# Performance work log

Measured on AMD Instinct MI355X. Metric: run time of the kernel, lower is better.

## Reference

```python
import jax, jax.numpy as jnp
import numpy as np

N = 100_000
E = 3_200_000
IN_DIM = 2
HID = 64
NUM_LAYERS = 3


def setup_inputs() -> dict:
    key = jax.random.key(0)
    ks = jax.random.split(key, 16)
    feat = jax.random.normal(ks[0], (N, IN_DIM), dtype=jnp.float32)
    src = jax.random.randint(ks[1], (E,), 0, N, dtype=jnp.int32)
    dst = jax.random.randint(ks[2], (E,), 0, N, dtype=jnp.int32)
    u_mask = jnp.zeros((N,), dtype=bool).at[jnp.arange(0, 10)].set(True)
    v_mask = jnp.zeros((N,), dtype=bool).at[jnp.arange(10, 20)].set(True)
    inp = {"feat": feat, "src": src, "dst": dst, "u_mask": u_mask, "v_mask": v_mask}
    dims = [IN_DIM] + [HID] * NUM_LAYERS
    ki = 3
    for l in range(NUM_LAYERS):
        d_in = dims[l]
        inp[f"W1_{l}"] = jax.random.normal(ks[ki], (d_in, HID), dtype=jnp.float32) * (1.0 / np.sqrt(d_in)); ki += 1
        inp[f"b1_{l}"] = jnp.zeros((HID,), dtype=jnp.float32)
        inp[f"W2_{l}"] = jax.random.normal(ks[ki], (HID, HID), dtype=jnp.float32) * (1.0 / np.sqrt(HID)); ki += 1
        inp[f"b2_{l}"] = jnp.zeros((HID,), dtype=jnp.float32)
    return inp


def _gin_layer(h, src, dst, W1, b1, W2, b2, n_nodes):
    # GINConv(sum, eps=0): h' = MLP(h + sum_{j->i} h_j)
    agg = jax.ops.segment_sum(h[src], dst, num_segments=n_nodes)  # [N, d]
    z = h + agg
    z = jax.nn.relu(z @ W1 + b1)
    z = z @ W2 + b2
    return jax.nn.relu(z)  # module applies relu after conv


def _masked_means(h, u_mask, v_mask):
    other_mask = ~(u_mask | v_mask)
    masks = jnp.stack([u_mask, v_mask, other_mask]).astype(h.dtype)  # [3, N]
    counts = masks.sum(axis=1)                                      # [3]
    sums = masks @ h                                                # [3, H]
    means = jnp.where(counts[:, None] > 0,
                      sums / jnp.maximum(counts, 1.0)[:, None],
                      jnp.zeros_like(sums))
    return means.reshape(-1)  # [3*H] = [h_u | h_v | h_other]


def reference(feat, src, dst, u_mask, v_mask,
              W1_0, b1_0, W2_0, b2_0,
              W1_1, b1_1, W2_1, b2_1,
              W1_2, b1_2, W2_2, b2_2):
    n_nodes = feat.shape[0]
    params = [(W1_0, b1_0, W2_0, b2_0), (W1_1, b1_1, W2_1, b2_1), (W1_2, b1_2, W2_2, b2_2)]
    h = feat
    parts = []
    for (W1, b1, W2, b2) in params:
        h = _gin_layer(h, src, dst, W1, b1, W2, b2, n_nodes)
        parts.append(_masked_means(h, u_mask, v_mask))
    return jnp.concatenate(parts)  # (num_layers * 3 * hidden_dim,)
```

## Files before the change

### kernel.cpp

```cpp
#include <hip/hip_runtime.h>

#define HID 64
#define G_LOG 7
#define G_SZ 128
#define NBKT_MAX 1024
#define STAGE_MAX 6144

typedef float f32x4 __attribute__((ext_vector_type(4)));
typedef short bf16x8 __attribute__((ext_vector_type(8)));

__device__ __forceinline__ float bf2f(unsigned int u) {
    union { unsigned int i; float f; } c; c.i = u << 16; return c.f;
}
__device__ __forceinline__ float bf2f_hi(unsigned int u) {
    union { unsigned int i; float f; } c; c.i = u & 0xFFFF0000u; return c.f;
}
__device__ __forceinline__ unsigned short f2bf(float f) {
    union { float f; unsigned int i; } c; c.f = f;
    unsigned int r = (c.i + 0x7FFFu + ((c.i >> 16) & 1u)) >> 16;
    return (unsigned short)r;
}
__device__ __forceinline__ unsigned int pack2(float a, float b) {
    return (unsigned int)f2bf(a) | ((unsigned int)f2bf(b) << 16);
}

__global__ void detect_mask_kernel(const unsigned char* __restrict__ u,
                                   int* __restrict__ flag)
{
    *flag = (u[1] != 0) ? 1 : 0;
}

__device__ __forceinline__ int mask_at(const void* m, int n, int is_u8)
{
    return is_u8 ? (((const unsigned char*)m)[n] != 0)
                 : (((const int*)m)[n] != 0);
}

__global__ __launch_bounds__(256) void count_masks_kernel(
    const void* __restrict__ u, const void* __restrict__ v,
    const int* __restrict__ flag, int* __restrict__ counts, int N)
{
    const int is_u8 = *flag;
    int tid = blockIdx.x * blockDim.x + threadIdx.x;
    int stride = gridDim.x * blockDim.x;
    int cu = 0, cv = 0, co = 0;
    for (int n = tid; n < N; n += stride) {
        int bu = mask_at(u, n, is_u8), bv = mask_at(v, n, is_u8);
        cu += bu; cv += bv; co += ((bu | bv) ^ 1);
    }
    atomicAdd(&counts[0], cu);
    atomicAdd(&counts[1], cv);
    atomicAdd(&counts[2], co);
}

__global__ __launch_bounds__(1024) void bucket_hist_kernel(
    const int* __restrict__ dst, int* __restrict__ bktCount, int E, int nbkt)
{
    __shared__ int lh[NBKT_MAX];
    const int bdim = blockDim.x;
    for (int i = threadIdx.x; i < nbkt; i += bdim) lh[i] = 0;
    __syncthreads();
    const int chunk = (E + gridDim.x - 1) / gridDim.x;
    const int c0 = blockIdx.x * chunk;
    const int c1 = min(E, c0 + chunk);
    for (int e = c0 + threadIdx.x; e < c1; e += bdim)
        atomicAdd(&lh[dst[e] >> G_LOG], 1);
    __syncthreads();
    for (int i = threadIdx.x; i < nbkt; i += bdim)
        if (lh[i]) atomicAdd(&bktCount[i], lh[i]);
}

__global__ __launch_bounds__(1024) void bucket_scan_kernel(
    const int* __restrict__ bktCount, int* __restrict__ bktBase,
    int* __restrict__ bktCursor, int nbkt)
{
    __shared__ int s[NBKT_MAX];
    const int t = threadIdx.x;
    int v = (t < nbkt) ? bktCount[t] : 0;
    s[t] = v;
    __syncthreads();
    for (int off = 1; off < NBKT_MAX; off <<= 1) {
        int x = (t >= off) ? s[t - off] : 0;
        __syncthreads();
        s[t] += x;
        __syncthreads();
    }
    if (t < nbkt) {
        int excl = s[t] - v;
        bktBase[t] = excl;
        bktCursor[t] = excl;
        if (t == nbkt - 1) bktBase[nbkt] = s[t];
    }
}

__global__ __launch_bounds__(1024) void binning_kernel(
    const int* __restrict__ src, const int* __restrict__ dst,
    int* __restrict__ bktCursor, unsigned int* __restrict__ packed,
    int E, int nbkt)
{
    __shared__ int lh[NBKT_MAX];
    __shared__ int lbase[NBKT_MAX];
    __shared__ int lcur[NBKT_MAX];
    const int bdim = blockDim.x;
    for (int i = threadIdx.x; i < nbkt; i += bdim) { lh[i] = 0; lcur[i] = 0; }
    __syncthreads();
    const int chunk = (E + gridDim.x - 1) / gridDim.x;
    const int c0 = blockIdx.x * chunk;
    const int c1 = min(E, c0 + chunk);
    for (int e = c0 + threadIdx.x; e < c1; e += bdim)
        atomicAdd(&lh[dst[e] >> G_LOG], 1);
    __syncthreads();
    for (int i = threadIdx.x; i < nbkt; i += bdim) {
        int h = lh[i];
        lbase[i] = h ? atomicAdd(&bktCursor[i], h) : 0;
    }
    __syncthreads();
    for (int e = c0 + threadIdx.x; e < c1; e += bdim) {
        int d = dst[e];
        int b = d >> G_LOG;
        int r = atomicAdd(&lcur[b], 1);
        packed[lbase[b] + r] =
            (unsigned int)src[e] | ((unsigned int)(d & (G_SZ - 1)) << 20);
    }
}

__global__ __launch_bounds__(512) void bucket_csr_kernel(
    const unsigned int* __restrict__ packed, const int* __restrict__ bktBase,
    int* __restrict__ row_ptr, int* __restrict__ csr_src, int N, int E)
{
    __shared__ int ncount[G_SZ];
    __shared__ int sc[G_SZ];
    __shared__ int ncur[G_SZ];
    __shared__ int stage[STAGE_MAX];
    const int b = blockIdx.x;
    const int t = threadIdx.x;
    const int bdim = blockDim.x;
    const int beg = bktBase[b], end = bktBase[b + 1];
    const int cnt = end - beg;

    if (t < G_SZ) ncount[t] = 0;
    __syncthreads();
    for (int i = beg + t; i < end; i += bdim)
        atomicAdd(&ncount[(packed[i] >> 20) & (G_SZ - 1)], 1);
    __syncthreads();
    if (t < G_SZ) sc[t] = ncount[t];
    __syncthreads();
    for (int off = 1; off < G_SZ; off <<= 1) {
        int x = 0;
        if (t < G_SZ && t >= off) x = sc[t - off];
        __syncthreads();
        if (t < G_SZ) sc[t] += x;
        __syncthreads();
    }
    if (t < G_SZ) {
        int excl = sc[t] - ncount[t];
        ncur[t] = excl;
        int node = (b << G_LOG) + t;
        if (node < N) row_ptr[node] = beg + excl;
    }
    if (b == 0 && t == 0) row_ptr[N] = E;
    __syncthreads();

    if (cnt <= STAGE_MAX) {
        for (int i = beg + t; i < end; i += bdim) {
            unsigned int p = packed[i];
            int dl = (p >> 20) & (G_SZ - 1);
            int r = atomicAdd(&ncur[dl], 1);
            stage[r] = (int)(p & 0xFFFFFu);
        }
        __syncthreads();
        for (int i = t; i < cnt; i += bdim) csr_src[beg + i] = stage[i];
    } else {
        for (int i = beg + t; i < end; i += bdim) {
            unsigned int p = packed[i];
            int dl = (p >> 20) & (G_SZ - 1);
            int r = atomicAdd(&ncur[dl], 1);
            csr_src[beg + r] = (int)(p & 0xFFFFFu);
        }
    }
}

__global__ __launch_bounds__(256) void gather64_kernel(
    const unsigned short* __restrict__ h, const int* __restrict__ row_ptr,
    const int* __restrict__ csr_src, unsigned short* __restrict__ agg, int N)
{
    const int lane = threadIdx.x & 63;
    const int slot = lane >> 3;
    const int chunk = lane & 7;
    const int wave = (blockIdx.x * blockDim.x + threadIdx.x) >> 6;
    const int nwaves = (gridDim.x * blockDim.x) >> 6;

    for (int n = wave; n < N; n += nwaves) {
        const int beg = row_ptr[n], end = row_ptr[n + 1];
        float a0[8], a1[8];
#pragma unroll
        for (int j = 0; j < 8; j++) { a0[j] = 0.0f; a1[j] = 0.0f; }

        int i = beg + slot;
        for (; i + 8 < end; i += 16) {
            int s0 = csr_src[i];
            int s1 = csr_src[i + 8];
            uint4 h0 = *reinterpret_cast<const uint4*>(h + (size_t)s0 * HID + chunk * 8);
            uint4 h1 = *reinterpret_cast<const uint4*>(h + (size_t)s1 * HID + chunk * 8);
            a0[0] += bf2f(h0.x & 0xFFFFu); a0[1] += bf2f_hi(h0.x);
            a0[2] += bf2f(h0.y & 0xFFFFu); a0[3] += bf2f_hi(h0.y);
            a0[4] += bf2f(h0.z & 0xFFFFu); a0[5] += bf2f_hi(h0.z);
            a0[6] += bf2f(h0.w & 0xFFFFu); a0[7] += bf2f_hi(h0.w);
            a1[0] += bf2f(h1.x & 0xFFFFu); a1[1] += bf2f_hi(h1.x);
            a1[2] += bf2f(h1.y & 0xFFFFu); a1[3] += bf2f_hi(h1.y);
            a1[4] += bf2f(h1.z & 0xFFFFu); a1[5] += bf2f_hi(h1.z);
            a1[6] += bf2f(h1.w & 0xFFFFu); a1[7] += bf2f_hi(h1.w);
        }
        if (i < end) {
            int s0 = csr_src[i];
            uint4 h0 = *reinterpret_cast<const uint4*>(h + (size_t)s0 * HID + chunk * 8);
            a0[0] += bf2f(h0.x & 0xFFFFu); a0[1] += bf2f_hi(h0.x);
            a0[2] += bf2f(h0.y & 0xFFFFu); a0[3] += bf2f_hi(h0.y);
            a0[4] += bf2f(h0.z & 0xFFFFu); a0[5] += bf2f_hi(h0.z);
            a0[6] += bf2f(h0.w & 0xFFFFu); a0[7] += bf2f_hi(h0.w);
        }
#pragma unroll
        for (int j = 0; j < 8; j++) a0[j] += a1[j];

#pragma unroll
        for (int off = 8; off < 64; off <<= 1) {
#pragma unroll
            for (int j = 0; j < 8; j++) a0[j] += __shfl_xor(a0[j], off, 64);
        }
        if (lane < 8) {
            unsigned int w0 = pack2(a0[0], a0[1]);
            unsigned int w1 = pack2(a0[2], a0[3]);
            unsigned int w2 = pack2(a0[4], a0[5]);
            unsigned int w3 = pack2(a0[6], a0[7]);
            uint4 o = {w0, w1, w2, w3};
            *reinterpret_cast<uint4*>(agg + (size_t)n * HID + lane * 8) = o;
        }
    }
}

__device__ __forceinline__ void load_wfrags(const float* __restrict__ W,
                                            int lg, int ln, bf16x8 wf[2][4])
{
#pragma unroll
    for (int kb = 0; kb < 2; kb++)
#pragma unroll
        for (int jb = 0; jb < 4; jb++) {
            bf16x8 w;
#pragma unroll
            for (int j = 0; j < 8; j++)
                w[j] = (short)f2bf(W[(kb * 32 + lg * 8 + j) * HID + jb * 16 + ln]);
            wf[kb][jb] = w;
        }
}

__device__ __forceinline__ bf16x8 zfrag_add(const unsigned short* __restrict__ h,
                                            const unsigned short* __restrict__ agg,
                                            size_t off)
{
    uint4 hv = *reinterpret_cast<const uint4*>(h + off);
    uint4 av = *reinterpret_cast<const uint4*>(agg + off);
    bf16x8 r;
    r[0] = (short)f2bf(bf2f(hv.x & 0xFFFFu) + bf2f(av.x & 0xFFFFu));
    r[1] = (short)f2bf(bf2f_hi(hv.x) + bf2f_hi(av.x));
    r[2] = (short)f2bf(bf2f(hv.y & 0xFFFFu) + bf2f(av.y & 0xFFFFu));
    r[3] = (short)f2bf(bf2f_hi(hv.y) + bf2f_hi(av.y));
    r[4] = (short)f2bf(bf2f(hv.z & 0xFFFFu) + bf2f(av.z & 0xFFFFu));
    r[5] = (short)f2bf(bf2f_hi(hv.z) + bf2f_hi(av.z));
    r[6] = (short)f2bf(bf2f(hv.w & 0xFFFFu) + bf2f(av.w & 0xFFFFu));
    r[7] = (short)f2bf(bf2f_hi(hv.w) + bf2f_hi(av.w));
    return r;
}

__global__ __launch_bounds__(256) void gin64_mfma_kernel(
    const unsigned short* __restrict__ h, const unsigned short* __restrict__ agg,
    const float* __restrict__ W1, const float* __restrict__ b1,
    const float* __restrict__ W2, const float* __restrict__ b2,
    unsigned short* __restrict__ out, int N)
{
    __shared__ __align__(16) unsigned short ytile[4][64 * 18];
    __shared__ __align__(16) unsigned short otile[4][16 * 72];

    const int lane = threadIdx.x & 63;
    const int wid = threadIdx.x >> 6;
    const int lg = lane >> 4, ln = lane & 15;

    bf16x8 w1f[2][4], w2f[2][4];
    load_wfrags(W1, lg, ln, w1f);
    load_wfrags(W2, lg, ln, w2f);
    float b1v[4], b2v[4];
#pragma unroll
    for (int jb = 0; jb < 4; jb++) {
        b1v[jb] = b1[jb * 16 + ln];
        b2v[jb] = b2[jb * 16 + ln];
    }

    const int nb = (blockIdx.x * 4 + wid) * 16;
    if (nb >= N) return;

    const int nodeA = min(nb + ln, N - 1);
    bf16x8 a0 = zfrag_add(h, agg, (size_t)nodeA * HID + 0 * 32 + lg * 8);
    bf16x8 a1 = zfrag_add(h, agg, (size_t)nodeA * HID + 1 * 32 + lg * 8);

    unsigned short* yt = ytile[wid];
#pragma unroll
    for (int jb = 0; jb < 4; jb++) {
        f32x4 acc = {0.f, 0.f, 0.f, 0.f};
        acc = __builtin_amdgcn_mfma_f32_16x16x32_bf16(a0, w1f[0][jb], acc, 0, 0, 0);
        acc = __builtin_amdgcn_mfma_f32_16x16x32_bf16(a1, w1f[1][jb], acc, 0, 0, 0);
#pragma unroll
        for (int r = 0; r < 4; r++) {
            float v = fmaxf(acc[r] + b1v[jb], 0.0f);
            yt[(jb * 16 + ln) * 18 + lg * 4 + r] = f2bf(v);
        }
    }
    __builtin_amdgcn_s_waitcnt(0);

    bf16x8 a2[2];
#pragma unroll
    for (int kb = 0; kb < 2; kb++) {
        bf16x8 t;
#pragma unroll
        for (int j = 0; j < 8; j++)
            t[j] = (short)yt[(kb * 32 + lg * 8 + j) * 18 + ln];
        a2[kb] = t;
    }

    unsigned short* ot = otile[wid];
#pragma unroll
    for (int jb = 0; jb < 4; jb++) {
        f32x4 acc = {0.f, 0.f, 0.f, 0.f};
        acc = __builtin_amdgcn_mfma_f32_16x16x32_bf16(a2[0], w2f[0][jb], acc, 0, 0, 0);
        acc = __builtin_amdgcn_mfma_f32_16x16x32_bf16(a2[1], w2f[1][jb], acc, 0, 0, 0);
#pragma unroll
        for (int r = 0; r < 4; r++) {
            float v = fmaxf(acc[r] + b2v[jb], 0.0f);
            ot[(lg * 4 + r) * 72 + jb * 16 + ln] = f2bf(v);
        }
    }
    __builtin_amdgcn_s_waitcnt(0);

    const int node2 = nb + (lane >> 2);
    if (node2 < N) {
        const unsigned short* sp = ot + (lane >> 2) * 72 + (lane & 3) * 16;
        uint4 o0 = *reinterpret_cast<const uint4*>(sp);
        uint4 o1 = *reinterpret_cast<const uint4*>(sp + 8);
        unsigned short* gp = out + (size_t)node2 * HID + (lane & 3) * 16;
        *reinterpret_cast<uint4*>(gp) = o0;
        *reinterpret_cast<uint4*>(gp + 8) = o1;
    }
}

__global__ __launch_bounds__(256) void mm64_relu_mfma_kernel(
    const unsigned short* __restrict__ in,
    const float* __restrict__ W, const float* __restrict__ b,
    unsigned short* __restrict__ out, int N)
{
    __shared__ __align__(16) unsigned short otile[4][16 * 72];

    const int lane = threadIdx.x & 63;
    const int wid = threadIdx.x >> 6;
    const int lg = lane >> 4, ln = lane & 15;

    bf16x8 wf[2][4];
    load_wfrags(W, lg, ln, wf);
    float bv[4];
#pragma unroll
    for (int jb = 0; jb < 4; jb++) bv[jb] = b[jb * 16 + ln];

    const int nb = (blockIdx.x * 4 + wid) * 16;
    if (nb >= N) return;

    const int nodeA = min(nb + ln, N - 1);
    bf16x8 a0 = *reinterpret_cast<const bf16x8*>(in + (size_t)nodeA * HID + 0 * 32 + lg * 8);
    bf16x8 a1 = *reinterpret_cast<const bf16x8*>(in + (size_t)nodeA * HID + 1 * 32 + lg * 8);

    unsigned short* ot = otile[wid];
#pragma unroll
    for (int jb = 0; jb < 4; jb++) {
        f32x4 acc = {0.f, 0.f, 0.f, 0.f};
        acc = __builtin_amdgcn_mfma_f32_16x16x32_bf16(a0, wf[0][jb], acc, 0, 0, 0);
        acc = __builtin_amdgcn_mfma_f32_16x16x32_bf16(a1, wf[1][jb], acc, 0, 0, 0);
#pragma unroll
        for (int r = 0; r < 4; r++) {
            float v = fmaxf(acc[r] + bv[jb], 0.0f);
            ot[(lg * 4 + r) * 72 + jb * 16 + ln] = f2bf(v);
        }
    }
    __builtin_amdgcn_s_waitcnt(0);

    const int node2 = nb + (lane >> 2);
    if (node2 < N) {
        const unsigned short* sp = ot + (lane >> 2) * 72 + (lane & 3) * 16;
        uint4 o0 = *reinterpret_cast<const uint4*>(sp);
        uint4 o1 = *reinterpret_cast<const uint4*>(sp + 8);
        unsigned short* gp = out + (size_t)node2 * HID + (lane & 3) * 16;
        *reinterpret_cast<uint4*>(gp) = o0;
        *reinterpret_cast<uint4*>(gp + 8) = o1;
    }
}

__global__ __launch_bounds__(256) void mlp2_y1_kernel(
    const float* __restrict__ feat, const int* __restrict__ row_ptr,
    const int* __restrict__ csr_src,
    const float* __restrict__ W1, const float* __restrict__ b1,
    unsigned short* __restrict__ out, int N)
{
    __shared__ float W1s[2 * HID];
    __shared__ float b1s[HID];
    const int tid = threadIdx.x;
    if (tid < 2 * HID) W1s[tid] = W1[tid];
    if (tid < HID) b1s[tid] = b1[tid];
    __syncthreads();

    const int stride = gridDim.x * 256;
    for (int node = blockIdx.x * 256 + tid; node < N; node += stride) {
        float2 f = *reinterpret_cast<const float2*>(&feat[(size_t)node * 2]);
        float z0 = f.x, z1 = f.y;
        const int beg = row_ptr[node], end = row_ptr[node + 1];
        int i = beg;
        for (; i + 3 < end; i += 4) {
            float2 g0 = *reinterpret_cast<const float2*>(&feat[(size_t)csr_src[i + 0] * 2]);
            float2 g1 = *reinterpret_cast<const float2*>(&feat[(size_t)csr_src[i + 1] * 2]);
            float2 g2 = *reinterpret_cast<const float2*>(&feat[(size_t)csr_src[i + 2] * 2]);
            float2 g3 = *reinterpret_cast<const float2*>(&feat[(size_t)csr_src[i + 3] * 2]);
            z0 += (g0.x + g1.x) + (g2.x + g3.x);
            z1 += (g0.y + g1.y) + (g2.y + g3.y);
        }
        for (; i < end; ++i) {
            float2 g = *reinterpret_cast<const float2*>(&feat[(size_t)csr_src[i] * 2]);
            z0 += g.x; z1 += g.y;
        }
        uint4* op = reinterpret_cast<uint4*>(out + (size_t)node * HID);
#pragma unroll
        for (int jc = 0; jc < 4; jc++) {
            unsigned int w[8];
#pragma unroll
            for (int p = 0; p < 8; p++) {
                int j0 = jc * 16 + 2 * p, j1 = j0 + 1;
                float v0 = fmaxf(b1s[j0] + z0 * W1s[j0] + z1 * W1s[HID + j0], 0.f);
                float v1 = fmaxf(b1s[j1] + z0 * W1s[j1] + z1 * W1s[HID + j1], 0.f);
                w[p] = pack2(v0, v1);
            }
            uint4 o0 = {w[0], w[1], w[2], w[3]};
            uint4 o1 = {w[4], w[5], w[6], w[7]};
            op[jc * 2 + 0] = o0;
            op[jc * 2 + 1] = o1;
        }
    }
}

__global__ __launch_bounds__(256) void masked_reduce_kernel(
    const unsigned short* __restrict__ h, const void* __restrict__ u,
    const void* __restrict__ v, const int* __restrict__ flag,
    float* __restrict__ sums, int N)
{
    __shared__ float ls[3][HID];
    const int tid = threadIdx.x;
    const int is_u8 = *flag;
    const int f8 = tid & 7;
    const int nloc = tid >> 3;

    if (tid < 3 * HID) ls[tid / HID][tid % HID] = 0.0f;
    __syncthreads();

    float su[8], sv[8], so[8];
#pragma unroll
    for (int j = 0; j < 8; j++) { su[j] = 0.f; sv[j] = 0.f; so[j] = 0.f; }

    for (int base = blockIdx.x * 32; base < N; base += gridDim.x * 32) {
        int n = base + nloc;
        if (n < N) {
            uint4 hv = *reinterpret_cast<const uint4*>(h + (size_t)n * HID + f8 * 8);
            float x[8];
            x[0] = bf2f(hv.x & 0xFFFFu); x[1] = bf2f_hi(hv.x);
            x[2] = bf2f(hv.y & 0xFFFFu); x[3] = bf2f_hi(hv.y);
            x[4] = bf2f(hv.z & 0xFFFFu); x[5] = bf2f_hi(hv.z);
            x[6] = bf2f(hv.w & 0xFFFFu); x[7] = bf2f_hi(hv.w);
            int bu = mask_at(u, n, is_u8), bv = mask_at(v, n, is_u8);
            if (bu) {
#pragma unroll
                for (int j = 0; j < 8; j++) su[j] += x[j];
            }
            if (bv) {
#pragma unroll
                for (int j = 0; j < 8; j++) sv[j] += x[j];
            }
            if (!(bu | bv)) {
#pragma unroll
                for (int j = 0; j < 8; j++) so[j] += x[j];
            }
        }
    }

#pragma unroll
    for (int off = 8; off < 64; off <<= 1) {
#pragma unroll
        for (int j = 0; j < 8; j++) {
            su[j] += __shfl_xor(su[j], off, 64);
            sv[j] += __shfl_xor(sv[j], off, 64);
            so[j] += __shfl_xor(so[j], off, 64);
        }
    }
    if ((tid & 63) < 8) {
        const int f0 = (tid & 7) * 8;
#pragma unroll
        for (int j = 0; j < 8; j++) {
            atomicAdd(&ls[0][f0 + j], su[j]);
            atomicAdd(&ls[1][f0 + j], sv[j]);
            atomicAdd(&ls[2][f0 + j], so[j]);
        }
    }
    __syncthreads();
    if (tid < 3 * HID) {
        float vsum = ls[tid / HID][tid % HID];
        if (vsum != 0.0f) atomicAdd(&sums[tid], vsum);
    }
}

__global__ void finalize_kernel(const float* __restrict__ sums,
                                const int* __restrict__ counts,
                                float* __restrict__ out)
{
    int i = blockIdx.x * blockDim.x + threadIdx.x;
    if (i >= 3 * 3 * HID) return;
    int g = (i / HID) % 3;
    float c = (float)counts[g];
    out[i] = (c > 0.0f) ? sums[i] / fmaxf(c, 1.0f) : 0.0f;
}

extern "C" void kernel_launch(void* const* d_in, const int* in_sizes, int n_in,
                              void* d_out, int out_size, void* d_ws, size_t ws_size,
                              hipStream_t stream)
{
    const float* feat = (const float*)d_in[0];
    const int* src = (const int*)d_in[1];
    const int* dst = (const int*)d_in[2];
    const void* um = d_in[3];
    const void* vm = d_in[4];
    const float* W1_0 = (const float*)d_in[5];
    const float* b1_0 = (const float*)d_in[6];
    const float* W2_0 = (const float*)d_in[7];
    const float* b2_0 = (const float*)d_in[8];
    const float* W1_1 = (const float*)d_in[9];
    const float* b1_1 = (const float*)d_in[10];
    const float* W2_1 = (const float*)d_in[11];
    const float* b2_1 = (const float*)d_in[12];
    const float* W1_2 = (const float*)d_in[13];
    const float* b1_2 = (const float*)d_in[14];
    const float* W2_2 = (const float*)d_in[15];
    const float* b2_2 = (const float*)d_in[16];

    const int N = in_sizes[0] / 2;
    const int E = in_sizes[1];
    const int nbkt = (N + G_SZ - 1) >> G_LOG;

    unsigned short* bufA = (unsigned short*)d_ws;
    unsigned short* bufB = bufA + (size_t)N * HID;
    unsigned short* bufC = bufB + (size_t)N * HID;
    unsigned int* packed = (unsigned int*)(bufC + (size_t)N * HID);
    int* csr_src = (int*)(packed + E);
    int* row_ptr = csr_src + E;
    int* bktCount = row_ptr + (N + 1);
    int* bktBase = bktCount + (NBKT_MAX + 1);
    int* bktCursor = bktBase + (NBKT_MAX + 1);
    float* sums = (float*)(bktCursor + NBKT_MAX);
    int* counts = (int*)(sums + 3 * 3 * HID);
    int* flag = counts + 3;

    const int mfma_grid = (N + 63) / 64;

    hipMemsetAsync(sums, 0, (3 * 3 * HID) * sizeof(float) + 3 * sizeof(int), stream);
    hipMemsetAsync(bktCount, 0, (NBKT_MAX + 1) * sizeof(int), stream);
    detect_mask_kernel<<<1, 1, 0, stream>>>((const unsigned char*)um, flag);
    count_masks_kernel<<<64, 256, 0, stream>>>(um, vm, flag, counts, N);

    bucket_hist_kernel<<<256, 1024, 0, stream>>>(dst, bktCount, E, nbkt);
    bucket_scan_kernel<<<1, 1024, 0, stream>>>(bktCount, bktBase, bktCursor, nbkt);
    binning_kernel<<<256, 1024, 0, stream>>>(src, dst, bktCursor, packed, E, nbkt);
    bucket_csr_kernel<<<nbkt, 512, 0, stream>>>(packed, bktBase, row_ptr, csr_src, N, E);

    mlp2_y1_kernel<<<(N + 255) / 256, 256, 0, stream>>>(feat, row_ptr, csr_src,
                                                        W1_0, b1_0, bufB, N);
    mm64_relu_mfma_kernel<<<mfma_grid, 256, 0, stream>>>(bufB, W2_0, b2_0, bufA, N);
    masked_reduce_kernel<<<512, 256, 0, stream>>>(bufA, um, vm, flag, sums + 0 * 3 * HID, N);

    gather64_kernel<<<2048, 256, 0, stream>>>(bufA, row_ptr, csr_src, bufB, N);
    gin64_mfma_kernel<<<mfma_grid, 256, 0, stream>>>(bufA, bufB, W1_1, b1_1,
                                                     W2_1, b2_1, bufC, N);
    masked_reduce_kernel<<<512, 256, 0, stream>>>(bufC, um, vm, flag, sums + 1 * 3 * HID, N);

    gather64_kernel<<<2048, 256, 0, stream>>>(bufC, row_ptr, csr_src, bufB, N);
    gin64_mfma_kernel<<<mfma_grid, 256, 0, stream>>>(bufC, bufB, W1_2, b1_2,
                                                     W2_2, b2_2, bufA, N);
    masked_reduce_kernel<<<512, 256, 0, stream>>>(bufA, um, vm, flag, sums + 2 * 3 * HID, N);

    finalize_kernel<<<1, 576, 0, stream>>>(sums, counts, (float*)d_out);
}
```

Before: 313.9 us.

## Stage binned edges in shared memory and write buckets contiguously

The binning kernel now computes a block-local exclusive scan of its per-bucket histogram and scatters the packed edges into a shared-memory staging buffer. Each wave then copies whole bucket runs to global memory in contiguous, coalesced writes instead of random per-edge scattered stores. The grid is now sized so each block's chunk fits the staging buffer, giving 250 blocks. The mlp2_y1 launch also changes to a fixed 2048 blocks, which only works correctly if that kernel uses a grid-stride loop. The trade-offs are about 65 KB of LDS per block, which limits occupancy, plus extra syncs for the scan.

```diff
diff --git a/kernel.cpp b/kernel.cpp
--- a/kernel.cpp
+++ b/kernel.cpp
@@ -5,6 +5,7 @@
 #define G_SZ 128
 #define NBKT_MAX 1024
 #define STAGE_MAX 6144
+#define BIN_STAGE 12800
 
 typedef float f32x4 __attribute__((ext_vector_type(4)));
 typedef short bf16x8 __attribute__((ext_vector_type(8)));
@@ -100,27 +101,55 @@
 {
     __shared__ int lh[NBKT_MAX];
     __shared__ int lbase[NBKT_MAX];
+    __shared__ int gbase[NBKT_MAX];
     __shared__ int lcur[NBKT_MAX];
+    __shared__ unsigned int staged[BIN_STAGE];
+
     const int bdim = blockDim.x;
-    for (int i = threadIdx.x; i < nbkt; i += bdim) { lh[i] = 0; lcur[i] = 0; }
-    __syncthreads();
+    const int t = threadIdx.x;
+    for (int i = t; i < nbkt; i += bdim) lh[i] = 0;
+    __syncthreads();
+
     const int chunk = (E + gridDim.x - 1) / gridDim.x;
     const int c0 = blockIdx.x * chunk;
     const int c1 = min(E, c0 + chunk);
-    for (int e = c0 + threadIdx.x; e < c1; e += bdim)
+
+    for (int e = c0 + t; e < c1; e += bdim)
         atomicAdd(&lh[dst[e] >> G_LOG], 1);
     __syncthreads();
-    for (int i = threadIdx.x; i < nbkt; i += bdim) {
-        int h = lh[i];
-        lbase[i] = h ? atomicAdd(&bktCursor[i], h) : 0;
-    }
-    __syncthreads();
-    for (int e = c0 + threadIdx.x; e < c1; e += bdim) {
+
+    int v = (t < nbkt) ? lh[t] : 0;
+    lbase[t] = v;
+    __syncthreads();
+    for (int off = 1; off < NBKT_MAX; off <<= 1) {
+        int x = (t >= off) ? lbase[t - off] : 0;
+        __syncthreads();
+        lbase[t] += x;
+        __syncthreads();
+    }
+    int excl = lbase[t] - v;
+    lbase[t] = excl;
+    lcur[t] = 0;
+    if (t < nbkt) gbase[t] = (v > 0) ? atomicAdd(&bktCursor[t], v) : 0;
+    __syncthreads();
+
+    for (int e = c0 + t; e < c1; e += bdim) {
         int d = dst[e];
         int b = d >> G_LOG;
         int r = atomicAdd(&lcur[b], 1);
-        packed[lbase[b] + r] =
+        staged[lbase[b] + r] =
             (unsigned int)src[e] | ((unsigned int)(d & (G_SZ - 1)) << 20);
+    }
+    __syncthreads();
+
+    const int wid = t >> 6;
+    const int lane = t & 63;
+    for (int b = wid; b < nbkt; b += 16) {
+        int cnt = lh[b];
+        int lb = lbase[b];
+        int gb = gbase[b];
+        for (int i = lane; i < cnt; i += 64)
+            packed[gb + i] = staged[lb + i];
     }
 }
 
@@ -568,6 +597,7 @@
     int* flag = counts + 3;
 
     const int mfma_grid = (N + 63) / 64;
+    const int bin_grid = (E + BIN_STAGE - 1) / BIN_STAGE;
 
     hipMemsetAsync(sums, 0, (3 * 3 * HID) * sizeof(float) + 3 * sizeof(int), stream);
     hipMemsetAsync(bktCount, 0, (NBKT_MAX + 1) * sizeof(int), stream);
@@ -576,11 +606,11 @@
 
     bucket_hist_kernel<<<256, 1024, 0, stream>>>(dst, bktCount, E, nbkt);
     bucket_scan_kernel<<<1, 1024, 0, stream>>>(bktCount, bktBase, bktCursor, nbkt);
-    binning_kernel<<<256, 1024, 0, stream>>>(src, dst, bktCursor, packed, E, nbkt);
+    binning_kernel<<<bin_grid, 1024, 0, stream>>>(src, dst, bktCursor, packed, E, nbkt);
     bucket_csr_kernel<<<nbkt, 512, 0, stream>>>(packed, bktBase, row_ptr, csr_src, N, E);
 
-    mlp2_y1_kernel<<<(N + 255) / 256, 256, 0, stream>>>(feat, row_ptr, csr_src,
-                                                        W1_0, b1_0, bufB, N);
+    mlp2_y1_kernel<<<2048, 256, 0, stream>>>(feat, row_ptr, csr_src,
+                                             W1_0, b1_0, bufB, N);
     mm64_relu_mfma_kernel<<<mfma_grid, 256, 0, stream>>>(bufB, W2_0, b2_0, bufA, N);
     masked_reduce_kernel<<<512, 256, 0, stream>>>(bufA, um, vm, flag, sums + 0 * 3 * HID, N);
 
```

Result: no change. 314.4 us (+0.2%).
